# Performance work log

Measured on AMD Instinct MI355X. Metric: run time of the kernel, lower is better.

Reference implementation:

```python
import jax, jax.numpy as jnp
import numpy as np

N, DIN, H, C, TD = 8192, 83, 256, 34, 16
NLAYERS, KNN, NSTEPS = 2, 11, 10  # KNN = k+1 with k=10
BN_EPS = 1e-5


def _lin(x, w, b):
    return x @ w + b


def setup_inputs() -> dict:
    ks = iter(jax.random.split(jax.random.key(0), 64))

    def W(*s):
        return jax.random.normal(next(ks), s, jnp.float32) / np.sqrt(s[-2]).astype(np.float32)

    def B(*s):
        return jax.random.normal(next(ks), s, jnp.float32) * 0.01

    return {
        "x": jax.random.normal(next(ks), (N, DIN), jnp.float32),
        "enc_w1": W(DIN, H), "enc_b1": B(H),
        "enc_w2": W(H, H), "enc_b2": B(H),
        "bn_g": jnp.ones((H,), jnp.float32), "bn_b": jnp.zeros((H,), jnp.float32),
        "bn_m": jnp.zeros((H,), jnp.float32), "bn_v": jnp.ones((H,), jnp.float32),
        "tg_node_w": W(NLAYERS, H, H), "tg_node_b": B(NLAYERS, H),
        "tg_t_w1": W(NLAYERS, 1, TD), "tg_t_b1": B(NLAYERS, TD),
        "tg_t_w2": W(NLAYERS, TD, H), "tg_t_b2": B(NLAYERS, H),
        "tg_gate_w": W(NLAYERS, 2 * H, H), "tg_gate_b": B(NLAYERS, H),
        "sde_w1": W(H + 1, H), "sde_b1": B(H),
        "sde_w2": W(H, H), "sde_b2": B(H),
        "sde_w3": W(H, H), "sde_b3": B(H),
        "dec_w1": W(H, H // 2), "dec_b1": B(H // 2),
        "dec_w2": W(H // 2, C), "dec_b2": B(C),
    }


def reference(x, enc_w1, enc_b1, enc_w2, enc_b2, bn_g, bn_b, bn_m, bn_v,
              tg_node_w, tg_node_b, tg_t_w1, tg_t_b1, tg_t_w2, tg_t_b2,
              tg_gate_w, tg_gate_b, sde_w1, sde_b1, sde_w2, sde_b2,
              sde_w3, sde_b3, dec_w1, dec_b1, dec_w2, dec_b2):
    # --- encoder (eval: dropout off, BatchNorm1d uses running stats) ---
    h = jax.nn.relu(_lin(x, enc_w1, enc_b1))
    h = jax.nn.relu(_lin(h, enc_w2, enc_b2))
    h = (h - bn_m) * jax.lax.rsqrt(bn_v + BN_EPS) * bn_g + bn_b

    # --- kNN graph from detached features ---
    hd = jax.lax.stop_gradient(h)
    hn = hd / jnp.maximum(jnp.linalg.norm(hd, axis=-1, keepdims=True), 1e-12)
    sim = hn @ hn.T                                    # [N, N]
    _, idx = jax.lax.top_k(sim, KNN)                   # [N, k+1]
    mask = jnp.zeros_like(sim).at[jnp.arange(sim.shape[0])[:, None], idx].set(1.0)
    adj = sim * mask
    adj = adj / jnp.maximum(adj.sum(-1, keepdims=True), 1.0)

    # --- temporal gated graph convolutions ---
    t = 0.0
    for l in range(NLAYERS):
        ht = _lin(h, tg_node_w[l], tg_node_b[l])       # node transform [N, H]
        agg = adj @ ht                                 # message aggregation
        tv = jnp.full((1, 1), t, h.dtype)
        te = _lin(jax.nn.relu(_lin(tv, tg_t_w1[l], tg_t_b1[l])), tg_t_w2[l], tg_t_b2[l])  # [1, H]
        gin = jnp.concatenate([agg, jnp.broadcast_to(te, agg.shape)], axis=-1)
        g = jax.nn.sigmoid(_lin(gin, tg_gate_w[l], tg_gate_b[l]))
        h = jax.nn.relu(g * agg + (1.0 - g) * ht)
        t += 0.5

    # --- eval-mode SDE: deterministic drift-only Euler steps ---
    dt = 1.0 / NSTEPS

    def step(hc, tc):
        hcat = jnp.concatenate([hc, jnp.full((hc.shape[0], 1), tc, hc.dtype)], axis=-1)
        d = jnp.tanh(_lin(hcat, sde_w1, sde_b1))
        d = jnp.tanh(_lin(d, sde_w2, sde_b2))
        d = jnp.tanh(_lin(d, sde_w3, sde_b3))
        return hc + d * dt, None

    ts = jnp.arange(NSTEPS, dtype=h.dtype) * dt
    h, _ = jax.lax.scan(step, h, ts)

    # --- decoder ---
    return _lin(jax.nn.relu(_lin(h, dec_w1, dec_b1)), dec_w2, dec_b2)
```

## Files before the change

kernel.cpp:

```cpp
#include <hip/hip_runtime.h>
#include <cmath>
#include <cstddef>

#define NROWS 8192
#define HDIM  256
#define KNN   11
#define NT    64
#define TS    128
#define TILE_ELEMS (TS*TS)
#define NTILES (NT*(NT+1)/2)

enum { EPI_NONE=0, EPI_RELU=1, EPI_TANH=3, EPI_GATE=4, EPI_SDE=5 };
enum { NPE_NONE=0, NPE_RELU=1, NPE_RELU_BN=2 };

__device__ __forceinline__ float add_rn(float a, float b){ float d; asm("v_add_f32 %0, %1, %2":"=v"(d):"v"(a),"v"(b)); return d; }
__device__ __forceinline__ float sub_rn(float a, float b){ float d; asm("v_sub_f32 %0, %1, %2":"=v"(d):"v"(a),"v"(b)); return d; }
__device__ __forceinline__ float mul_rn(float a, float b){ float d; asm("v_mul_f32 %0, %1, %2":"=v"(d):"v"(a),"v"(b)); return d; }

__device__ __host__ __forceinline__ size_t tidx(int br, int bc)
{
    return (size_t)br * NT - (size_t)br * (br - 1) / 2 + (size_t)(bc - br);
}

__device__ __forceinline__ float epi_apply(int EPI, float z, int gn,
    const float* bias, const float* bn_m, const float* bn_r,
    const float* bn_g, const float* bn_b)
{
    if (EPI == NPE_NONE) return z;
    z = add_rn(z, bias[gn]);
    z = fmaxf(z, 0.f);
    if (EPI == NPE_RELU) return z;
    z = sub_rn(z, bn_m[gn]);
    z = mul_rn(z, bn_r[gn]);
    z = mul_rn(z, bn_g[gn]);
    z = add_rn(z, bn_b[gn]);
    return z;
}

template<int EPI, bool TRANSB>
__global__ __launch_bounds__(256)
void gemm_ma2(const float* __restrict__ A, int lda,
              const float* __restrict__ B, int ldb,
              const float* __restrict__ bias,
              float* __restrict__ C, int ldc,
              int M, int N, int K,
              const float* __restrict__ bn_m, const float* __restrict__ bn_r,
              const float* __restrict__ bn_g, const float* __restrict__ bn_b)
{
    __shared__ float As[32][132];
    __shared__ float Bs[32][132];
    const int tid = threadIdx.x;
    const int tx = tid & 15, ty = tid >> 4;
    const int m0 = blockIdx.y * 128, n0 = blockIdx.x * 128;

    float acc[8][8];
    #pragma unroll
    for (int i = 0; i < 8; ++i)
        #pragma unroll
        for (int j = 0; j < 8; ++j) acc[i][j] = 0.f;

    for (int kc = 0; kc < K; kc += 32) {
        #pragma unroll
        for (int u = 0; u < 16; ++u) {
            int idx = tid + u * 256;
            int kk = idx & 31, m = idx >> 5;
            int gm = m0 + m, gk = kc + kk;
            As[kk][m] = (gm < M && gk < K) ? A[(size_t)gm * lda + gk] : 0.f;
        }
        #pragma unroll
        for (int u = 0; u < 16; ++u) {
            int idx = tid + u * 256;
            if (TRANSB) {
                int kk = idx & 31, n = idx >> 5;
                int gn = n0 + n, gk = kc + kk;
                Bs[kk][n] = (gn < N && gk < K) ? B[(size_t)gn * ldb + gk] : 0.f;
            } else {
                int n = idx & 127, kk = idx >> 7;
                int gn = n0 + n, gk = kc + kk;
                Bs[kk][n] = (gk < K && gn < N) ? B[(size_t)gk * ldb + gn] : 0.f;
            }
        }
        __syncthreads();
        #pragma unroll
        for (int kk = 0; kk < 32; ++kk) {
            float4 a0 = *(const float4*)&As[kk][ty * 8];
            float4 a1 = *(const float4*)&As[kk][ty * 8 + 4];
            float4 b0 = *(const float4*)&Bs[kk][tx * 8];
            float4 b1 = *(const float4*)&Bs[kk][tx * 8 + 4];
            float a[8] = {a0.x,a0.y,a0.z,a0.w,a1.x,a1.y,a1.z,a1.w};
            float b[8] = {b0.x,b0.y,b0.z,b0.w,b1.x,b1.y,b1.z,b1.w};
            #pragma unroll
            for (int i = 0; i < 8; ++i)
                #pragma unroll
                for (int j = 0; j < 8; ++j)
                    acc[i][j] = add_rn(acc[i][j], mul_rn(a[i], b[j]));
        }
        __syncthreads();
    }

    #pragma unroll
    for (int i = 0; i < 8; ++i) {
        int gm = m0 + ty * 8 + i;
        if (gm >= M) continue;
        #pragma unroll
        for (int j = 0; j < 8; ++j) {
            int gn = n0 + tx * 8 + j;
            if (gn >= N) continue;
            C[(size_t)gm * ldc + gn] = epi_apply(EPI, acc[i][j], gn, bias, bn_m, bn_r, bn_g, bn_b);
        }
    }
}

__global__ __launch_bounds__(256)
void gemm_sim_sym_packed(const float* __restrict__ hn, float* __restrict__ P)
{
    size_t t = blockIdx.x;
    int br = 0;
    while ((size_t)(br + 1) * NT - (size_t)(br + 1) * br / 2 <= t) ++br;
    int bc = br + (int)(t - ((size_t)br * NT - (size_t)br * (br - 1) / 2));

    __shared__ float As[32][132];
    __shared__ float Bs[32][132];
    const int tid = threadIdx.x;
    const int tx = tid & 15, ty = tid >> 4;
    const int m0 = br * 128, n0 = bc * 128;

    float acc[8][8];
    #pragma unroll
    for (int i = 0; i < 8; ++i)
        #pragma unroll
        for (int j = 0; j < 8; ++j) acc[i][j] = 0.f;

    #pragma unroll 1
    for (int kc = 0; kc < HDIM; kc += 32) {
        #pragma unroll
        for (int u = 0; u < 16; ++u) {
            int idx = tid + u * 256;
            int kk = idx & 31, m = idx >> 5;
            As[kk][m] = hn[(size_t)(m0 + m) * HDIM + kc + kk];
            Bs[kk][m] = hn[(size_t)(n0 + m) * HDIM + kc + kk];
        }
        __syncthreads();
        #pragma unroll
        for (int kk = 0; kk < 32; ++kk) {
            float4 a0 = *(const float4*)&As[kk][ty * 8];
            float4 a1 = *(const float4*)&As[kk][ty * 8 + 4];
            float4 b0 = *(const float4*)&Bs[kk][tx * 8];
            float4 b1 = *(const float4*)&Bs[kk][tx * 8 + 4];
            float a[8] = {a0.x,a0.y,a0.z,a0.w,a1.x,a1.y,a1.z,a1.w};
            float b[8] = {b0.x,b0.y,b0.z,b0.w,b1.x,b1.y,b1.z,b1.w};
            #pragma unroll
            for (int i = 0; i < 8; ++i)
                #pragma unroll
                for (int j = 0; j < 8; ++j)
                    acc[i][j] = add_rn(acc[i][j], mul_rn(a[i], b[j]));
        }
        __syncthreads();
    }

    float* tile = P + t * TILE_ELEMS;
    #pragma unroll
    for (int i = 0; i < 8; ++i) {
        float* tr = tile + (size_t)(ty * 8 + i) * TS + tx * 8;
        #pragma unroll
        for (int j = 0; j < 8; ++j) tr[j] = acc[i][j];
    }
}

__global__ void bn_prep_np(const float* __restrict__ v, float* __restrict__ r)
{
    int i = threadIdx.x;
    float vpe = add_rn(v[i], 1e-5f);
    r[i] = 1.0f / sqrtf(vpe);
}

__global__ __launch_bounds__(256)
void rownorm_np2(const float* __restrict__ h, float* __restrict__ hn)
{
    int r = blockIdx.x * 256 + threadIdx.x;
    if (r >= NROWS) return;
    const float* x = h + (size_t)r * HDIM;
    float tot = 0.f;
    #pragma unroll
    for (int half = 0; half < 2; ++half) {
        const float* a = x + half * 128;
        float rr[8];
        #pragma unroll
        for (int jj = 0; jj < 8; ++jj) rr[jj] = mul_rn(a[jj], a[jj]);
        #pragma unroll 1
        for (int ii = 8; ii < 128; ii += 8) {
            #pragma unroll
            for (int jj = 0; jj < 8; ++jj) rr[jj] = add_rn(rr[jj], mul_rn(a[ii + jj], a[ii + jj]));
        }
        float blk = add_rn(add_rn(add_rn(rr[0], rr[1]), add_rn(rr[2], rr[3])),
                           add_rn(add_rn(rr[4], rr[5]), add_rn(rr[6], rr[7])));
        tot = (half == 0) ? blk : add_rn(tot, blk);
    }
    float den = fmaxf(sqrtf(tot), 1e-12f);
    float* o = hn + (size_t)r * HDIM;
    for (int ii = 0; ii < HDIM; ++ii) o[ii] = x[ii] / den;
}

__device__ __forceinline__ void ins11(float (&av)[KNN], int (&ai)[KNN], float v, int vi)
{
    if (v > av[KNN - 1]) {
        #pragma unroll
        for (int j = 0; j < KNN; ++j) {
            bool better = (v > av[j]);
            float tv = better ? av[j] : v;  int ti = better ? ai[j] : vi;
            av[j] = better ? v : av[j];     ai[j] = better ? vi : ai[j];
            v = tv; vi = ti;
        }
    }
}

__global__ __launch_bounds__(256)
void topk_wave_sym(const float* __restrict__ P,
                   int* __restrict__ idx_out, float* __restrict__ wgt_out)
{
    __shared__ float colbuf[4][132];
    const int tid = threadIdx.x;
    const int w = tid >> 6;
    const int lane = tid & 63;
    const int wid0 = blockIdx.x * 4;
    const int wid = wid0 + w;
    const int br = wid >> 7, rr = wid & 127;
    const int rr0 = wid0 & 127;

    float av[KNN]; int ai[KNN];
    #pragma unroll
    for (int j = 0; j < KNN; ++j) { av[j] = -3.402823e38f; ai[j] = 0x7fffffff; }

    #pragma unroll 1
    for (int cb = 0; cb < NT; ++cb) {
        int c0 = cb * TS + lane * 2;
        if (cb >= br) {
            const float* tile = P + tidx(br, cb) * TILE_ELEMS;
            float2 v2 = *(const float2*)&tile[(size_t)rr * TS + lane * 2];
            ins11(av, ai, v2.x, c0);
            ins11(av, ai, v2.y, c0 + 1);
        } else {
            const float* tile = P + tidx(cb, br) * TILE_ELEMS;
            __syncthreads();
            if (tid < 128) {
                float4 v4 = *(const float4*)&tile[(size_t)tid * TS + rr0];
                colbuf[0][tid] = v4.x; colbuf[1][tid] = v4.y;
                colbuf[2][tid] = v4.z; colbuf[3][tid] = v4.w;
            }
            __syncthreads();
            float va = colbuf[w][lane * 2];
            float vb = colbuf[w][lane * 2 + 1];
            ins11(av, ai, va, c0);
            ins11(av, ai, vb, c0 + 1);
        }
    }

    #pragma unroll 1
    for (int m = 1; m < 64; m <<= 1) {
        float bv[KNN]; int bi[KNN];
        #pragma unroll
        for (int j = 0; j < KNN; ++j) {
            bv[j] = __shfl_xor(av[j], m, 64);
            bi[j] = __shfl_xor(ai[j], m, 64);
        }
        #pragma unroll
        for (int j = 0; j < KNN; ++j) {
            float v = bv[j]; int vi = bi[j];
            bool enter = (v > av[KNN - 1]) || (v == av[KNN - 1] && vi < ai[KNN - 1]);
            if (enter) {
                #pragma unroll
                for (int q = 0; q < KNN; ++q) {
                    bool better = (v > av[q]) || (v == av[q] && vi < ai[q]);
                    float tv = better ? av[q] : v;  int ti = better ? ai[q] : vi;
                    av[q] = better ? v : av[q];     ai[q] = better ? vi : ai[q];
                    v = tv; vi = ti;
                }
            }
        }
    }

    if (lane == 0) {
        double s = 0.0;
        #pragma unroll
        for (int j = 0; j < KNN; ++j) s += (double)av[j];
        double den = fmax(s, 1.0);
        #pragma unroll
        for (int j = 0; j < KNN; ++j) {
            idx_out[(size_t)wid * KNN + j] = ai[j];
            wgt_out[(size_t)wid * KNN + j] = (float)((double)av[j] / den);
        }
    }
}

__global__ __launch_bounds__(256)
void topk_wave(const float* __restrict__ sim, int r0, int R,
               int* __restrict__ idx_out, float* __restrict__ wgt_out)
{
    const int wid = blockIdx.x * 4 + (threadIdx.x >> 6);
    const int lane = threadIdx.x & 63;
    if (wid >= R) return;
    const float* row = sim + (size_t)wid * NROWS;

    float av[KNN]; int ai[KNN];
    #pragma unroll
    for (int j = 0; j < KNN; ++j) { av[j] = -3.402823e38f; ai[j] = 0x7fffffff; }

    #pragma unroll 1
    for (int it = 0; it < NROWS / 256; ++it) {
        float4 v4 = *(const float4*)&row[lane * 4 + it * 256];
        float vv[4] = {v4.x, v4.y, v4.z, v4.w};
        #pragma unroll
        for (int q = 0; q < 4; ++q)
            ins11(av, ai, vv[q], lane * 4 + it * 256 + q);
    }

    #pragma unroll 1
    for (int m = 1; m < 64; m <<= 1) {
        float bv[KNN]; int bi[KNN];
        #pragma unroll
        for (int j = 0; j < KNN; ++j) {
            bv[j] = __shfl_xor(av[j], m, 64);
            bi[j] = __shfl_xor(ai[j], m, 64);
        }
        #pragma unroll
        for (int j = 0; j < KNN; ++j) {
            float v = bv[j]; int vi = bi[j];
            bool enter = (v > av[KNN - 1]) || (v == av[KNN - 1] && vi < ai[KNN - 1]);
            if (enter) {
                #pragma unroll
                for (int q = 0; q < KNN; ++q) {
                    bool better = (v > av[q]) || (v == av[q] && vi < ai[q]);
                    float tv = better ? av[q] : v;  int ti = better ? ai[q] : vi;
                    av[q] = better ? v : av[q];     ai[q] = better ? vi : ai[q];
                    v = tv; vi = ti;
                }
            }
        }
    }

    if (lane == 0) {
        double s = 0.0;
        #pragma unroll
        for (int j = 0; j < KNN; ++j) s += (double)av[j];
        double den = fmax(s, 1.0);
        int gr = r0 + wid;
        #pragma unroll
        for (int j = 0; j < KNN; ++j) {
            idx_out[(size_t)gr * KNN + j] = ai[j];
            wgt_out[(size_t)gr * KNN + j] = (float)((double)av[j] / den);
        }
    }
}

#define SROWS 16
#define SSTR  (HDIM + 4)

__device__ __forceinline__ void sde_layer(
    const float (*in)[SSTR], float (*out)[SSTR],
    const float* __restrict__ W, const float* __restrict__ bias,
    const float* __restrict__ tw, float t, int rg, int cg)
{
    __syncthreads();
    float acc[4][4];
    #pragma unroll
    for (int i = 0; i < 4; ++i)
        #pragma unroll
        for (int j = 0; j < 4; ++j) acc[i][j] = 0.f;

    #pragma unroll 1
    for (int k = 0; k < HDIM; k += 4) {
        float4 a4[4];
        #pragma unroll
        for (int i = 0; i < 4; ++i) a4[i] = *(const float4*)&in[rg * 4 + i][k];
        float4 w4[4];
        #pragma unroll
        for (int q = 0; q < 4; ++q) w4[q] = *(const float4*)&W[(size_t)(k + q) * HDIM + cg * 4];
        #pragma unroll
        for (int i = 0; i < 4; ++i) {
            float avv[4] = {a4[i].x, a4[i].y, a4[i].z, a4[i].w};
            #pragma unroll
            for (int q = 0; q < 4; ++q) {
                acc[i][0] = __builtin_fmaf(avv[q], w4[q].x, acc[i][0]);
                acc[i][1] = __builtin_fmaf(avv[q], w4[q].y, acc[i][1]);
                acc[i][2] = __builtin_fmaf(avv[q], w4[q].z, acc[i][2]);
                acc[i][3] = __builtin_fmaf(avv[q], w4[q].w, acc[i][3]);
            }
        }
    }

    float bb[4];
    #pragma unroll
    for (int j = 0; j < 4; ++j) {
        bb[j] = bias[cg * 4 + j];
        if (tw) bb[j] += t * tw[cg * 4 + j];
    }
    #pragma unroll
    for (int i = 0; i < 4; ++i)
        #pragma unroll
        for (int j = 0; j < 4; ++j)
            out[rg * 4 + i][cg * 4 + j] = tanhf(acc[i][j] + bb[j]);
}

__global__ __launch_bounds__(256)
void sde_fused(const float* __restrict__ w1, const float* __restrict__ b1,
               const float* __restrict__ w2, const float* __restrict__ b2,
               const float* __restrict__ w3, const float* __restrict__ b3,
               float* __restrict__ h)
{
    __shared__ float hs[SROWS][SSTR];
    __shared__ float bufA[SROWS][SSTR];
    __shared__ float bufB[SROWS][SSTR];
    const int tid = threadIdx.x;
    const int r0 = blockIdx.x * SROWS;
    const int rg = tid >> 6;
    const int cg = tid & 63;

    for (int i = tid; i < SROWS * HDIM; i += 256) {
        int r = i >> 8, c = i & 255;
        hs[r][c] = h[(size_t)(r0 + r) * HDIM + c];
    }

    #pragma unroll 1
    for (int s = 0; s < 10; ++s) {
        float t = 0.1f * (float)s;
        sde_layer(hs,  bufA, w1, b1, w1 + (size_t)HDIM * HDIM, t, rg, cg);
        sde_layer(bufA, bufB, w2, b2, nullptr, 0.f, rg, cg);
        sde_layer(bufB, bufA, w3, b3, nullptr, 0.f, rg, cg);
        __syncthreads();
        for (int i = tid; i < SROWS * HDIM; i += 256) {
            int r = i >> 8, c = i & 255;
            hs[r][c] += 0.1f * bufA[r][c];
        }
    }
    __syncthreads();
    for (int i = tid; i < SROWS * HDIM; i += 256) {
        int r = i >> 8, c = i & 255;
        h[(size_t)(r0 + r) * HDIM + c] = hs[r][c];
    }
}

template<int EPI, bool TRANSB>
__global__ __launch_bounds__(256)
void gemm_f32(const float* __restrict__ A, int lda,
              const float* __restrict__ B, int ldb,
              const float* __restrict__ bias, const float* __restrict__ bias2, float bcoef,
              float* __restrict__ C, int ldc,
              int M, int N, int K,
              const float* __restrict__ E1, const float* __restrict__ E2, float coef)
{
    __shared__ float As[16][64];
    __shared__ float Bs[16][64];
    const int tid = threadIdx.x;
    const int tx = tid & 15, ty = tid >> 4;
    const int m0 = blockIdx.y * 64, n0 = blockIdx.x * 64;

    float acc[4][4] = {{0.f}};

    for (int k0 = 0; k0 < K; k0 += 16) {
        #pragma unroll
        for (int u = 0; u < 4; ++u) {
            int i = tid + u * 256;
            int kk = i & 15, m = i >> 4;
            int gm = m0 + m, gk = k0 + kk;
            As[kk][m] = (gm < M && gk < K) ? A[(size_t)gm * lda + gk] : 0.f;
        }
        if (!TRANSB) {
            #pragma unroll
            for (int u = 0; u < 4; ++u) {
                int i = tid + u * 256;
                int n = i & 63, kk = i >> 6;
                int gk = k0 + kk, gn = n0 + n;
                Bs[kk][n] = (gk < K && gn < N) ? B[(size_t)gk * ldb + gn] : 0.f;
            }
        } else {
            #pragma unroll
            for (int u = 0; u < 4; ++u) {
                int i = tid + u * 256;
                int kk = i & 15, n = i >> 4;
                int gk = k0 + kk, gn = n0 + n;
                Bs[kk][n] = (gk < K && gn < N) ? B[(size_t)gn * ldb + gk] : 0.f;
            }
        }
        __syncthreads();
        #pragma unroll
        for (int kk = 0; kk < 16; ++kk) {
            float4 avv = *(const float4*)&As[kk][ty * 4];
            float4 bvv = *(const float4*)&Bs[kk][tx * 4];
            float a[4] = {avv.x, avv.y, avv.z, avv.w};
            float b[4] = {bvv.x, bvv.y, bvv.z, bvv.w};
            #pragma unroll
            for (int i2 = 0; i2 < 4; ++i2)
                #pragma unroll
                for (int j = 0; j < 4; ++j)
                    acc[i2][j] += a[i2] * b[j];
        }
        __syncthreads();
    }

    #pragma unroll
    for (int i2 = 0; i2 < 4; ++i2) {
        int gm = m0 + ty * 4 + i2;
        if (gm >= M) continue;
        #pragma unroll
        for (int j = 0; j < 4; ++j) {
            int gn = n0 + tx * 4 + j;
            if (gn >= N) continue;
            float z = acc[i2][j];
            if (bias)  z += bias[gn];
            if (bias2) z += bcoef * bias2[gn];
            float r;
            if constexpr (EPI == EPI_NONE) {
                r = z;
            } else if constexpr (EPI == EPI_RELU) {
                r = fmaxf(z, 0.f);
            } else if constexpr (EPI == EPI_TANH) {
                r = tanhf(z);
            } else if constexpr (EPI == EPI_GATE) {
                float g = 1.f / (1.f + expf(-z));
                float avv = E1[(size_t)gm * ldc + gn];
                float hvv = E2[(size_t)gm * ldc + gn];
                r = fmaxf(g * avv + (1.f - g) * hvv, 0.f);
            } else {
                r = E1[(size_t)gm * ldc + gn] + tanhf(z) * coef;
            }
            C[(size_t)gm * ldc + gn] = r;
        }
    }
}

__global__ __launch_bounds__(256)
void gather_agg(const float* __restrict__ ht, const int* __restrict__ idx,
                const float* __restrict__ wgt, float* __restrict__ agg)
{
    int r = blockIdx.x, tid = threadIdx.x;
    __shared__ int   si[KNN];
    __shared__ float sw[KNN];
    if (tid < KNN) { si[tid] = idx[(size_t)r * KNN + tid]; sw[tid] = wgt[(size_t)r * KNN + tid]; }
    __syncthreads();
    float acc = 0.f;
    #pragma unroll
    for (int j = 0; j < KNN; ++j) acc += sw[j] * ht[(size_t)si[j] * HDIM + tid];
    agg[(size_t)r * HDIM + tid] = acc;
}

__global__ __launch_bounds__(256)
void te_gbias(const float* __restrict__ w1, const float* __restrict__ b1,
              const float* __restrict__ w2, const float* __restrict__ b2,
              const float* __restrict__ gw, const float* __restrict__ gb,
              float t, float* __restrict__ gbias)
{
    __shared__ float hid[16];
    __shared__ float te[256];
    int tid = threadIdx.x;
    if (tid < 16) hid[tid] = fmaxf(t * w1[tid] + b1[tid], 0.f);
    __syncthreads();
    float acc = b2[tid];
    #pragma unroll
    for (int i = 0; i < 16; ++i) acc += hid[i] * w2[i * 256 + tid];
    te[tid] = acc;
    __syncthreads();
    float g = gb[tid];
    for (int j = 0; j < 256; ++j) g += te[j] * gw[j * 256 + tid];
    gbias[tid] = g;
}

extern "C" void kernel_launch(void* const* d_in, const int* in_sizes, int n_in,
                              void* d_out, int out_size, void* d_ws, size_t ws_size,
                              hipStream_t stream)
{
    (void)in_sizes; (void)n_in; (void)out_size;
    const float* x       = (const float*)d_in[0];
    const float* enc_w1  = (const float*)d_in[1];
    const float* enc_b1  = (const float*)d_in[2];
    const float* enc_w2  = (const float*)d_in[3];
    const float* enc_b2  = (const float*)d_in[4];
    const float* bn_g    = (const float*)d_in[5];
    const float* bn_b    = (const float*)d_in[6];
    const float* bn_m    = (const float*)d_in[7];
    const float* bn_v    = (const float*)d_in[8];
    const float* tg_node_w = (const float*)d_in[9];
    const float* tg_node_b = (const float*)d_in[10];
    const float* tg_t_w1 = (const float*)d_in[11];
    const float* tg_t_b1 = (const float*)d_in[12];
    const float* tg_t_w2 = (const float*)d_in[13];
    const float* tg_t_b2 = (const float*)d_in[14];
    const float* tg_gate_w = (const float*)d_in[15];
    const float* tg_gate_b = (const float*)d_in[16];
    const float* sde_w1  = (const float*)d_in[17];
    const float* sde_b1  = (const float*)d_in[18];
    const float* sde_w2  = (const float*)d_in[19];
    const float* sde_b2  = (const float*)d_in[20];
    const float* sde_w3  = (const float*)d_in[21];
    const float* sde_b3  = (const float*)d_in[22];
    const float* dec_w1  = (const float*)d_in[23];
    const float* dec_b1  = (const float*)d_in[24];
    const float* dec_w2  = (const float*)d_in[25];
    const float* dec_b2  = (const float*)d_in[26];
    float* out = (float*)d_out;

    const size_t NH = (size_t)NROWS * HDIM;
    const size_t NK = (size_t)NROWS * KNN;
    const size_t PACKED_BYTES = (size_t)NTILES * TILE_ELEMS * 4;

    char* p = (char*)d_ws;
    float* h    = (float*)p;  p += NH * 4;
    float* hn   = (float*)p;  p += NH * 4;
    float* t1   = (float*)p;  p += NH * 4;
    float* t2   = (float*)p;  p += NH * 4;
    int*   ki   = (int*)p;    p += NK * 4;
    float* kw   = (float*)p;  p += NK * 4;
    float* bn_r   = (float*)p; p += 256 * 4;
    float* gbias  = (float*)p; p += 256 * 4;
    p += (16 - ((uintptr_t)p & 15)) & 15;
    float* simw = (float*)p;

    size_t used_bytes = (size_t)(p - (char*)d_ws);
    size_t availB = (ws_size > used_bytes) ? ws_size - used_bytes : 0;
    bool packed = (availB >= PACKED_BYTES);

    int chunk = 128;
    if (!packed) {
        long long avail2 = (long long)availB;
        chunk = (avail2 > 0) ? (int)(avail2 / ((long long)NROWS * 4)) : 128;
        if (chunk > NROWS) chunk = NROWS;
        chunk &= ~127;
        if (chunk < 128) chunk = 128;
    }

    dim3 blk(256);
    dim3 g64(4, NROWS / 64);
    dim3 g128(2, NROWS / 128);

    bn_prep_np<<<1, 256, 0, stream>>>(bn_v, bn_r);

    gemm_ma2<NPE_RELU, false><<<g128, blk, 0, stream>>>(
        x, 83, enc_w1, 256, enc_b1, t1, 256, NROWS, 256, 83, nullptr, nullptr, nullptr, nullptr);
    gemm_ma2<NPE_RELU_BN, false><<<g128, blk, 0, stream>>>(
        t1, 256, enc_w2, 256, enc_b2, h, 256, NROWS, 256, 256, bn_m, bn_r, bn_g, bn_b);
    rownorm_np2<<<NROWS / 256, 256, 0, stream>>>(h, hn);

    if (packed) {
        gemm_sim_sym_packed<<<NTILES, blk, 0, stream>>>(hn, simw);
        topk_wave_sym<<<NROWS / 4, 256, 0, stream>>>(simw, ki, kw);
    } else {
        for (int r0 = 0; r0 < NROWS; r0 += chunk) {
            int R = NROWS - r0; if (R > chunk) R = chunk;
            gemm_ma2<NPE_NONE, true><<<dim3(NROWS / 128, (R + 127) / 128), blk, 0, stream>>>(
                hn + (size_t)r0 * HDIM, HDIM, hn, HDIM, nullptr,
                simw, NROWS, R, NROWS, HDIM, nullptr, nullptr, nullptr, nullptr);
            topk_wave<<<(R + 3) / 4, 256, 0, stream>>>(simw, r0, R, ki, kw);
        }
    }

    float tval = 0.f;
    for (int l = 0; l < 2; ++l) {
        te_gbias<<<1, 256, 0, stream>>>(
            tg_t_w1 + l * 16, tg_t_b1 + l * 16,
            tg_t_w2 + (size_t)l * 16 * 256, tg_t_b2 + l * 256,
            tg_gate_w + ((size_t)l * 512 + 256) * 256, tg_gate_b + l * 256,
            tval, gbias);
        gemm_f32<EPI_NONE, false><<<g64, blk, 0, stream>>>(
            h, 256, tg_node_w + (size_t)l * 256 * 256, 256,
            tg_node_b + l * 256, nullptr, 0.f, t1, 256, NROWS, 256, 256,
            nullptr, nullptr, 0.f);
        gather_agg<<<NROWS, 256, 0, stream>>>(t1, ki, kw, t2);
        gemm_f32<EPI_GATE, false><<<g64, blk, 0, stream>>>(
            t2, 256, tg_gate_w + (size_t)l * 512 * 256, 256,
            gbias, nullptr, 0.f, h, 256, NROWS, 256, 256,
            t2, t1, 0.f);
        tval += 0.5f;
    }

    sde_fused<<<NROWS / SROWS, 256, 0, stream>>>(
        sde_w1, sde_b1, sde_w2, sde_b2, sde_w3, sde_b3, h);

    gemm_f32<EPI_RELU, false><<<dim3(2, NROWS / 64), blk, 0, stream>>>(
        h, 256, dec_w1, 128, dec_b1, nullptr, 0.f, t1, 128, NROWS, 128, 256,
        nullptr, nullptr, 0.f);
    gemm_f32<EPI_NONE, false><<<dim3(1, NROWS / 64), blk, 0, stream>>>(
        t1, 128, dec_w2, 34, dec_b2, nullptr, 0.f, out, 34, NROWS, 34, 128,
        nullptr, nullptr, 0.f);
}
```

Measured before the change: 2.095 ms.

## Split symmetric top-k into direct, mirrored-tile, and merge kernels

Replaces the single symmetric top-k kernel with three passes. Rows scan their own upper-triangle tiles, a per-tile kernel transposes off-diagonal tiles through shared memory to get column-wise candidates, and a final kernel merges the per-block-row candidate lists. The goal is to remove the strided column reads and per-iteration block syncs of the old lower-triangle path. The cost is extra candidate buffers in the workspace, a larger packed threshold, and two extra launches. It also makes tie-breaking by index consistent throughout.

```diff
diff --git a/kernel.cpp b/kernel.cpp
--- a/kernel.cpp
+++ b/kernel.cpp
@@ -9,6 +9,7 @@
 #define TS    128
 #define TILE_ELEMS (TS*TS)
 #define NTILES (NT*(NT+1)/2)
+#define CSTR  (NT*KNN)
 
 enum { EPI_NONE=0, EPI_RELU=1, EPI_TANH=3, EPI_GATE=4, EPI_SDE=5 };
 enum { NPE_NONE=0, NPE_RELU=1, NPE_RELU_BN=2 };
@@ -35,6 +36,19 @@
     z = mul_rn(z, bn_g[gn]);
     z = add_rn(z, bn_b[gn]);
     return z;
+}
+
+__device__ __forceinline__ void ins11f(float (&av)[KNN], int (&ai)[KNN], float v, int vi)
+{
+    if (v > av[KNN - 1] || (v == av[KNN - 1] && vi < ai[KNN - 1])) {
+        #pragma unroll
+        for (int j = 0; j < KNN; ++j) {
+            bool better = (v > av[j]) || (v == av[j] && vi < ai[j]);
+            float tv = better ? av[j] : v;  int ti = better ? ai[j] : vi;
+            av[j] = better ? v : av[j];     ai[j] = better ? vi : ai[j];
+            v = tv; vi = ti;
+        }
+    }
 }
 
 template<int EPI, bool TRANSB>
@@ -167,6 +181,148 @@
     }
 }
 
+__global__ __launch_bounds__(256)
+void topk_direct(const float* __restrict__ P,
+                 float* __restrict__ cv, int* __restrict__ ci)
+{
+    const int wid = blockIdx.x * 4 + (threadIdx.x >> 6);
+    const int lane = threadIdx.x & 63;
+    const int br = wid >> 7, rr = wid & 127;
+
+    float av[KNN]; int ai[KNN];
+    #pragma unroll
+    for (int j = 0; j < KNN; ++j) { av[j] = -3.402823e38f; ai[j] = 0x7fffffff; }
+
+    #pragma unroll 1
+    for (int cb = br; cb < NT; ++cb) {
+        const float* tile = P + tidx(br, cb) * TILE_ELEMS;
+        float2 v2 = *(const float2*)&tile[(size_t)rr * TS + lane * 2];
+        int c0 = cb * TS + lane * 2;
+        ins11f(av, ai, v2.x, c0);
+        ins11f(av, ai, v2.y, c0 + 1);
+    }
+
+    #pragma unroll 1
+    for (int m = 1; m < 64; m <<= 1) {
+        float bv[KNN]; int bi[KNN];
+        #pragma unroll
+        for (int j = 0; j < KNN; ++j) {
+            bv[j] = __shfl_xor(av[j], m, 64);
+            bi[j] = __shfl_xor(ai[j], m, 64);
+        }
+        #pragma unroll
+        for (int j = 0; j < KNN; ++j)
+            ins11f(av, ai, bv[j], bi[j]);
+    }
+
+    if (lane == 0) {
+        #pragma unroll
+        for (int j = 0; j < KNN; ++j) {
+            cv[(size_t)wid * CSTR + br * KNN + j] = av[j];
+            ci[(size_t)wid * CSTR + br * KNN + j] = ai[j];
+        }
+    }
+}
+
+__global__ __launch_bounds__(256)
+void topk_mirror(const float* __restrict__ P,
+                 float* __restrict__ cv, int* __restrict__ ci)
+{
+    size_t t = blockIdx.x;
+    int a = 0;
+    while ((size_t)(a + 1) * NT - (size_t)(a + 1) * a / 2 <= t) ++a;
+    int b = a + (int)(t - ((size_t)a * NT - (size_t)a * (a - 1) / 2));
+    if (a == b) return;
+
+    __shared__ float TT[TS][66];
+    const int tid = threadIdx.x;
+    const float* tile = P + t * TILE_ELEMS;
+
+    float av[KNN]; int ai[KNN];
+    #pragma unroll
+    for (int j = 0; j < KNN; ++j) { av[j] = -3.402823e38f; ai[j] = 0x7fffffff; }
+    const int c = tid & 127;
+
+    #pragma unroll 1
+    for (int half = 0; half < 2; ++half) {
+        int rstart = half * 64;
+        __syncthreads();
+        {
+            int r = rstart + (tid >> 2), cq = tid & 3;
+            const float* rowp = tile + (size_t)r * TS + cq * 32;
+            #pragma unroll
+            for (int q = 0; q < 8; ++q) {
+                float4 v4 = *(const float4*)&rowp[q * 4];
+                int cc = cq * 32 + q * 4;
+                TT[cc + 0][r - rstart] = v4.x;
+                TT[cc + 1][r - rstart] = v4.y;
+                TT[cc + 2][r - rstart] = v4.z;
+                TT[cc + 3][r - rstart] = v4.w;
+            }
+        }
+        __syncthreads();
+        if (tid < 128) {
+            #pragma unroll 4
+            for (int rl = 0; rl < 64; ++rl)
+                ins11f(av, ai, TT[c][rl], a * TS + rstart + rl);
+        }
+    }
+
+    if (tid < 128) {
+        int row = b * TS + c;
+        #pragma unroll
+        for (int j = 0; j < KNN; ++j) {
+            cv[(size_t)row * CSTR + a * KNN + j] = av[j];
+            ci[(size_t)row * CSTR + a * KNN + j] = ai[j];
+        }
+    }
+}
+
+__global__ __launch_bounds__(256)
+void topk_merge_b(const float* __restrict__ cv, const int* __restrict__ ci,
+                  int* __restrict__ idx_out, float* __restrict__ wgt_out)
+{
+    const int wid = blockIdx.x * 4 + (threadIdx.x >> 6);
+    const int lane = threadIdx.x & 63;
+    const int br = wid >> 7;
+
+    float av[KNN]; int ai[KNN];
+    if (lane <= br) {
+        const float* v = cv + (size_t)wid * CSTR + lane * KNN;
+        const int*   x = ci + (size_t)wid * CSTR + lane * KNN;
+        #pragma unroll
+        for (int j = 0; j < KNN; ++j) { av[j] = v[j]; ai[j] = x[j]; }
+    } else {
+        #pragma unroll
+        for (int j = 0; j < KNN; ++j) { av[j] = -3.402823e38f; ai[j] = 0x7fffffff; }
+    }
+
+    #pragma unroll 1
+    for (int m = 1; m < 64; m <<= 1) {
+        float bv[KNN]; int bi[KNN];
+        #pragma unroll
+        for (int j = 0; j < KNN; ++j) {
+            bv[j] = __shfl_xor(av[j], m, 64);
+            bi[j] = __shfl_xor(ai[j], m, 64);
+        }
+        #pragma unroll
+        for (int j = 0; j < KNN; ++j)
+            ins11f(av, ai, bv[j], bi[j]);
+    }
+
+    if (lane == 0) {
+        double s = 0.0;
+        #pragma unroll
+        for (int j = 0; j < KNN; ++j) s += (double)av[j];
+        double den = fmax(s, 1.0);
+        #pragma unroll
+        for (int j = 0; j < KNN; ++j) {
+            idx_out[(size_t)wid * KNN + j] = ai[j];
+            wgt_out[(size_t)wid * KNN + j] = (float)((double)av[j] / den);
+        }
+    }
+}
+
 __global__ void bn_prep_np(const float* __restrict__ v, float* __restrict__ r)
 {
     int i = threadIdx.x;
@@ -201,97 +357,6 @@
     for (int ii = 0; ii < HDIM; ++ii) o[ii] = x[ii] / den;
 }
 
-__device__ __forceinline__ void ins11(float (&av)[KNN], int (&ai)[KNN], float v, int vi)
-{
-    if (v > av[KNN - 1]) {
-        #pragma unroll
-        for (int j = 0; j < KNN; ++j) {
-            bool better = (v > av[j]);
-            float tv = better ? av[j] : v;  int ti = better ? ai[j] : vi;
-            av[j] = better ? v : av[j];     ai[j] = better ? vi : ai[j];
-            v = tv; vi = ti;
-        }
-    }
-}
-
-__global__ __launch_bounds__(256)
-void topk_wave_sym(const float* __restrict__ P,
-                   int* __restrict__ idx_out, float* __restrict__ wgt_out)
-{
-    __shared__ float colbuf[4][132];
-    const int tid = threadIdx.x;
-    const int w = tid >> 6;
-    const int lane = tid & 63;
-    const int wid0 = blockIdx.x * 4;
-    const int wid = wid0 + w;
-    const int br = wid >> 7, rr = wid & 127;
-    const int rr0 = wid0 & 127;
-
-    float av[KNN]; int ai[KNN];
-    #pragma unroll
-    for (int j = 0; j < KNN; ++j) { av[j] = -3.402823e38f; ai[j] = 0x7fffffff; }
-
-    #pragma unroll 1
-    for (int cb = 0; cb < NT; ++cb) {
-        int c0 = cb * TS + lane * 2;
-        if (cb >= br) {
-            const float* tile = P + tidx(br, cb) * TILE_ELEMS;
-            float2 v2 = *(const float2*)&tile[(size_t)rr * TS + lane * 2];
-            ins11(av, ai, v2.x, c0);
-            ins11(av, ai, v2.y, c0 + 1);
-        } else {
-            const float* tile = P + tidx(cb, br) * TILE_ELEMS;
-            __syncthreads();
-            if (tid < 128) {
-                float4 v4 = *(const float4*)&tile[(size_t)tid * TS + rr0];
-                colbuf[0][tid] = v4.x; colbuf[1][tid] = v4.y;
-                colbuf[2][tid] = v4.z; colbuf[3][tid] = v4.w;
-            }
-            __syncthreads();
-            float va = colbuf[w][lane * 2];
-            float vb = colbuf[w][lane * 2 + 1];
-            ins11(av, ai, va, c0);
-            ins11(av, ai, vb, c0 + 1);
-        }
-    }
-
-    #pragma unroll 1
-    for (int m = 1; m < 64; m <<= 1) {
-        float bv[KNN]; int bi[KNN];
-        #pragma unroll
-        for (int j = 0; j < KNN; ++j) {
-            bv[j] = __shfl_xor(av[j], m, 64);
-            bi[j] = __shfl_xor(ai[j], m, 64);
-        }
-        #pragma unroll
-        for (int j = 0; j < KNN; ++j) {
-            float v = bv[j]; int vi = bi[j];
-            bool enter = (v > av[KNN - 1]) || (v == av[KNN - 1] && vi < ai[KNN - 1]);
-            if (enter) {
-                #pragma unroll
-                for (int q = 0; q < KNN; ++q) {
-                    bool better = (v > av[q]) || (v == av[q] && vi < ai[q]);
-                    float tv = better ? av[q] : v;  int ti = better ? ai[q] : vi;
-                    av[q] = better ? v : av[q];     ai[q] = better ? vi : ai[q];
-                    v = tv; vi = ti;
-                }
-            }
-        }
-    }
-
-    if (lane == 0) {
-        double s = 0.0;
-        #pragma unroll
-        for (int j = 0; j < KNN; ++j) s += (double)av[j];
-        double den = fmax(s, 1.0);
-        #pragma unroll
-        for (int j = 0; j < KNN; ++j) {
-            idx_out[(size_t)wid * KNN + j] = ai[j];
-            wgt_out[(size_t)wid * KNN + j] = (float)((double)av[j] / den);
-        }
-    }
-}
-
 __global__ __launch_bounds__(256)
 void topk_wave(const float* __restrict__ sim, int r0, int R,
                int* __restrict__ idx_out, float* __restrict__ wgt_out)
@@ -311,7 +376,7 @@
         float vv[4] = {v4.x, v4.y, v4.z, v4.w};
         #pragma unroll
         for (int q = 0; q < 4; ++q)
-            ins11(av, ai, vv[q], lane * 4 + it * 256 + q);
+            ins11f(av, ai, vv[q], lane * 4 + it * 256 + q);
     }
 
     #pragma unroll 1
@@ -323,19 +388,8 @@
             bi[j] = __shfl_xor(ai[j], m, 64);
         }
         #pragma unroll
-        for (int j = 0; j < KNN; ++j) {
-            float v = bv[j]; int vi = bi[j];
-            bool enter = (v > av[KNN - 1]) || (v == av[KNN - 1] && vi < ai[KNN - 1]);
-            if (enter) {
-                #pragma unroll
-                for (int q = 0; q < KNN; ++q) {
-                    bool better = (v > av[q]) || (v == av[q] && vi < ai[q]);
-                    float tv = better ? av[q] : v;  int ti = better ? ai[q] : vi;
-                    av[q] = better ? v : av[q];     ai[q] = better ? vi : ai[q];
-                    v = tv; vi = ti;
-                }
-            }
-        }
+        for (int j = 0; j < KNN; ++j)
+            ins11f(av, ai, bv[j], bi[j]);
     }
 
     if (lane == 0) {
@@ -600,7 +654,8 @@
 
     const size_t NH = (size_t)NROWS * HDIM;
     const size_t NK = (size_t)NROWS * KNN;
-    const size_t PACKED_BYTES = (size_t)NTILES * TILE_ELEMS * 4;
+    const size_t PACKED_BYTES = (size_t)NTILES * TILE_ELEMS * 4
+                              + 2 * (size_t)NROWS * CSTR * 4;
 
     char* p = (char*)d_ws;
     float* h    = (float*)p;  p += NH * 4;
@@ -618,6 +673,9 @@
     size_t availB = (ws_size > used_bytes) ? ws_size - used_bytes : 0;
     bool packed = (availB >= PACKED_BYTES);
 
+    float* cv = simw + (size_t)NTILES * TILE_ELEMS;
+    int*   ci = (int*)(cv + (size_t)NROWS * CSTR);
+
     int chunk = 128;
     if (!packed) {
         long long avail2 = (long long)availB;
@@ -641,7 +699,9 @@
 
     if (packed) {
         gemm_sim_sym_packed<<<NTILES, blk, 0, stream>>>(hn, simw);
-        topk_wave_sym<<<NROWS / 4, 256, 0, stream>>>(simw, ki, kw);
+        topk_direct<<<NROWS / 4, 256, 0, stream>>>(simw, cv, ci);
+        topk_mirror<<<NTILES, 256, 0, stream>>>(simw, cv, ci);
+        topk_merge_b<<<NROWS / 4, 256, 0, stream>>>(cv, ci, ki, kw);
     } else {
         for (int r0 = 0; r0 < NROWS; r0 += chunk) {
             int R = NROWS - r0; if (R > chunk) R = chunk;
```

Result: slower. 2.343 ms (+11.8%).
